# Optimization experiments

Hardware: AMD Instinct MI355X
Metric: run time of the kernel (lower is better)

The kernel has to match this reference:

```python
import jax, jax.numpy as jnp
import numpy as np

B, S, D, H = 4, 2048, 1024, 16
DK = D // H  # 64
EPS = 1e-6


def setup_inputs() -> dict:
    key = jax.random.key(0)
    ks = jax.random.split(key, 8)
    scale = 0.02
    return {
        "query": jax.random.normal(ks[0], (B, S, D), jnp.float32),
        "key": jax.random.normal(ks[1], (B, S, D), jnp.float32),
        "value": jax.random.normal(ks[2], (B, S, D), jnp.float32),
        "mask": jnp.zeros((B, 1, S, S), jnp.float32),  # additive mask
        "Wq": jax.random.normal(ks[3], (D, D), jnp.float32) * scale,
        "Wk": jax.random.normal(ks[4], (D, D), jnp.float32) * scale,
        "Wv": jax.random.normal(ks[5], (D, D), jnp.float32) * scale,
        "Wo": jax.random.normal(ks[6], (D, D), jnp.float32) * scale,
        "gamma": jnp.ones((D,), jnp.float32),
        "beta": jnp.zeros((D,), jnp.float32),
    }


def reference(query, key, value, mask, Wq, Wk, Wv, Wo, gamma, beta):
    residual = query
    # projections: [B,S,D] -> [B,H,S,dk]
    q = (query @ Wq).reshape(B, S, H, DK).transpose(0, 2, 1, 3)
    k = (key @ Wk).reshape(B, S, H, DK).transpose(0, 2, 1, 3)
    v = (value @ Wv).reshape(B, S, H, DK).transpose(0, 2, 1, 3)
    temperature = jnp.sqrt(jnp.asarray(DK, q.dtype))
    scores = jnp.einsum("bhqd,bhkd->bhqk", q, k) / temperature + mask
    p_attn = jax.nn.softmax(scores, axis=-1)  # dropout p=0 (eval)
    x = jnp.einsum("bhqk,bhkd->bhqd", p_attn, v)
    x = x.transpose(0, 2, 1, 3).reshape(B, S, D)
    x = x @ Wo
    y = residual + x
    mu = jnp.mean(y, axis=-1, keepdims=True)
    var = jnp.var(y, axis=-1, keepdims=True)
    return (y - mu) * jax.lax.rsqrt(var + EPS) * gamma + beta
```

## Files before the change

### kernel.cpp

```cpp
#include <hip/hip_runtime.h>
#include <string.h>

typedef unsigned short u16;
typedef __bf16 bf16x8 __attribute__((ext_vector_type(8)));
typedef float f32x4 __attribute__((ext_vector_type(4)));
typedef u16 us8 __attribute__((ext_vector_type(8)));
typedef u16 us4 __attribute__((ext_vector_type(4)));

#define DEVINL __device__ __forceinline__

static constexpr int Bn = 4, Sn = 2048, Dn = 1024, Hn = 16;
static constexpr float LOG2E = 1.4426950408889634f;

DEVINL u16 f2bf(float f) {
  __bf16 h = (__bf16)f;
  u16 u;
  memcpy(&u, &h, 2);
  return u;
}

DEVINL void gload16(const void* g, void* l) {
  __builtin_amdgcn_global_load_lds((const __attribute__((address_space(1))) void*)g,
                                   (__attribute__((address_space(3))) void*)l, 16, 0, 0);
}

DEVINL unsigned swz(unsigned row, unsigned kbyte) {
  return row * 128u + (kbyte ^ ((row & 7u) << 4));
}

DEVINL bf16x8 lds8(const u16* base, unsigned byteoff) {
  return *(const bf16x8*)((const char*)base + byteoff);
}

__global__ __launch_bounds__(256) void cvt_all(const float* __restrict__ q, const float* __restrict__ k,
                                               const float* __restrict__ v, const float* __restrict__ mask,
                                               u16* __restrict__ oq, u16* __restrict__ ok,
                                               u16* __restrict__ ov, int* __restrict__ flag) {
  int z = blockIdx.y;
  if (z == 3) {
    size_t i = ((size_t)blockIdx.x * 256 + threadIdx.x) * 4;
    float4 m = *(const float4*)(mask + i);
    bool nz = (m.x != 0.f) || (m.y != 0.f) || (m.z != 0.f) || (m.w != 0.f);
    if (nz) atomicOr(flag, 1);
    return;
  }
  const float* in = z == 0 ? q : (z == 1 ? k : v);
  u16* out = z == 0 ? oq : (z == 1 ? ok : ov);
  size_t i = ((size_t)blockIdx.x * 256 + threadIdx.x) * 8;
  float4 a = *(const float4*)(in + i);
  float4 b = *(const float4*)(in + i + 4);
  us8 o;
  o[0] = f2bf(a.x); o[1] = f2bf(a.y); o[2] = f2bf(a.z); o[3] = f2bf(a.w);
  o[4] = f2bf(b.x); o[5] = f2bf(b.y); o[6] = f2bf(b.z); o[7] = f2bf(b.w);
  *(us8*)(out + i) = o;
}

__global__ __launch_bounds__(256) void cvt_w_all(const float* __restrict__ w0, const float* __restrict__ w1,
                                                 const float* __restrict__ w2, const float* __restrict__ w3,
                                                 u16* __restrict__ t0, u16* __restrict__ t1,
                                                 u16* __restrict__ t2, u16* __restrict__ t3) {
  int z = blockIdx.z;
  const float* W = z == 0 ? w0 : (z == 1 ? w1 : (z == 2 ? w2 : w3));
  u16* Wt = z == 0 ? t0 : (z == 1 ? t1 : (z == 2 ? t2 : t3));
  __shared__ float T[32][33];
  int n0 = blockIdx.x * 32, k0 = blockIdx.y * 32;
  int tx = threadIdx.x & 31, ty = threadIdx.x >> 5;
#pragma unroll
  for (int r = 0; r < 4; r++)
    T[ty + r * 8][tx] = W[(size_t)(k0 + ty + r * 8) * 1024 + n0 + tx];
  __syncthreads();
#pragma unroll
  for (int r = 0; r < 4; r++)
    Wt[(size_t)(n0 + ty + r * 8) * 1024 + k0 + tx] = f2bf(T[tx][ty + r * 8]);
}

__global__ __launch_bounds__(256) void transpose_v(const u16* __restrict__ V, u16* __restrict__ Vt) {
  __shared__ u16 T[64][72];
  int s0 = blockIdx.x * 64;
  int b = blockIdx.y >> 4, h = blockIdx.y & 15;
  int tid = threadIdx.x;
#pragma unroll
  for (int it = 0; it < 2; it++) {
    int chunk = it * 256 + tid;
    int s = chunk >> 3, c = chunk & 7;
    us8 v = *(const us8*)&V[((size_t)(b * Sn + s0 + s)) * Dn + h * 64 + c * 8];
#pragma unroll
    for (int j = 0; j < 8; j++) T[c * 8 + j][s] = v[j];
  }
  __syncthreads();
#pragma unroll
  for (int it = 0; it < 2; it++) {
    int chunk = it * 256 + tid;
    int dk = chunk >> 3, c = chunk & 7;
    us8 o;
#pragma unroll
    for (int jj = 0; jj < 8; jj++) o[jj] = T[dk][(jj & 3) * 16 + c * 2 + (jj >> 2)];
    *(us8*)&Vt[((size_t)((b * Hn + h) * 64 + dk)) * Sn + s0 + c * 8] = o;
  }
}

template <int EPI>
DEVINL void gemm_body(const u16* __restrict__ A, const u16* __restrict__ Bt, void* __restrict__ Cout,
                      const float* __restrict__ resid, float alpha, u16* As, u16* Bs, int m0, int n0) {
  constexpr int K = 1024, N = 1024;
  int tid = threadIdx.x, w = tid >> 6, l = tid & 63;
  int wr = w >> 1, wc = w & 1;
  int l15 = l & 15, l4 = l >> 4;
  int lrow8 = l >> 3;
  int chunk = (l & 7) ^ (lrow8 & 7);

  f32x4 acc[4][4];
#pragma unroll
  for (int i = 0; i < 4; i++)
#pragma unroll
    for (int j = 0; j < 4; j++)
#pragma unroll
      for (int r = 0; r < 4; r++) acc[i][j][r] = 0.f;

  for (int kt = 0; kt < K; kt += 64) {
    __syncthreads();
#pragma unroll
    for (int c = 0; c < 4; c++) {
      int rowb = w * 32 + c * 8;
      int row = rowb + lrow8;
      gload16(&A[(size_t)(m0 + row) * K + kt + chunk * 8], &As[rowb * 64]);
      gload16(&Bt[(size_t)(n0 + row) * K + kt + chunk * 8], &Bs[rowb * 64]);
    }
    __syncthreads();
#pragma unroll
    for (int kk = 0; kk < 2; kk++) {
      bf16x8 af[4], bfr[4];
#pragma unroll
      for (int i = 0; i < 4; i++) {
        af[i] = lds8(As, swz(wr * 64 + i * 16 + l15, kk * 64 + l4 * 16));
        bfr[i] = lds8(Bs, swz(wc * 64 + i * 16 + l15, kk * 64 + l4 * 16));
      }
#pragma unroll
      for (int mi = 0; mi < 4; mi++)
#pragma unroll
        for (int ni = 0; ni < 4; ni++)
          acc[mi][ni] = __builtin_amdgcn_mfma_f32_16x16x32_bf16(af[mi], bfr[ni], acc[mi][ni], 0, 0, 0);
    }
  }

#pragma unroll
  for (int mi = 0; mi < 4; mi++)
#pragma unroll
    for (int ni = 0; ni < 4; ni++)
#pragma unroll
      for (int r = 0; r < 4; r++) {
        int row = m0 + wr * 64 + mi * 16 + l4 * 4 + r;
        int col = n0 + wc * 64 + ni * 16 + l15;
        float v = acc[mi][ni][r] * alpha;
        if constexpr (EPI == 0) {
          ((u16*)Cout)[(size_t)row * N + col] = f2bf(v);
        } else {
          ((float*)Cout)[(size_t)row * N + col] = v + resid[(size_t)row * N + col];
        }
      }
}

DEVINL void swizzled_tiles(int& m0, int& n0) {
  int lin = blockIdx.y * 8 + blockIdx.x;
  int sl = (lin & 7) * 64 + (lin >> 3);
  n0 = (sl & 7) * 128;
  m0 = (sl >> 3) * 128;
}

__global__ __launch_bounds__(256) void gemm_qkv(const u16* __restrict__ Aq, const u16* __restrict__ Ak,
                                                const u16* __restrict__ Av, const u16* __restrict__ Wtq,
                                                const u16* __restrict__ Wtk, const u16* __restrict__ Wtv,
                                                u16* __restrict__ Cq, u16* __restrict__ Ck,
                                                u16* __restrict__ Cv, float alphaq) {
  __shared__ u16 As[128 * 64];
  __shared__ u16 Bs[128 * 64];
  int z = blockIdx.z;
  const u16* A = z == 0 ? Aq : (z == 1 ? Ak : Av);
  const u16* Bt = z == 0 ? Wtq : (z == 1 ? Wtk : Wtv);
  u16* C = z == 0 ? Cq : (z == 1 ? Ck : Cv);
  float alpha = z == 0 ? alphaq : 1.0f;
  int m0, n0;
  swizzled_tiles(m0, n0);
  gemm_body<0>(A, Bt, C, nullptr, alpha, As, Bs, m0, n0);
}

__global__ __launch_bounds__(256) void gemm_o(const u16* __restrict__ A, const u16* __restrict__ Bt,
                                              float* __restrict__ Cout, const float* __restrict__ resid) {
  __shared__ u16 As[128 * 64];
  __shared__ u16 Bs[128 * 64];
  int m0, n0;
  swizzled_tiles(m0, n0);
  gemm_body<1>(A, Bt, Cout, resid, 1.0f, As, Bs, m0, n0);
}

__global__ __launch_bounds__(256) void attn_k(const u16* __restrict__ Qb, const u16* __restrict__ Kb,
                                              const u16* __restrict__ Vt, const float* __restrict__ mask,
                                              const int* __restrict__ flag, u16* __restrict__ Ob) {
  __shared__ u16 Ks[2][64 * 64];
  __shared__ u16 Vs[2][64 * 64];
  __shared__ u16 Pl[4 * 32 * 72];
  int tid = threadIdx.x, w = tid >> 6, l = tid & 63;
  int l15 = l & 15, l4 = l >> 4;
  int b = blockIdx.y >> 4, h = blockIdx.y & 15;
  int q0 = blockIdx.x * 128;
  int lrow8 = l >> 3;
  int chunk = (l & 7) ^ (lrow8 & 7);

  bf16x8 qf[2][2];
#pragma unroll
  for (int mi = 0; mi < 2; mi++)
#pragma unroll
    for (int kk = 0; kk < 2; kk++) {
      int row = q0 + w * 32 + mi * 16 + l15;
      qf[mi][kk] = *(const bf16x8*)&Qb[((size_t)(b * Sn + row)) * Dn + h * 64 + kk * 32 + l4 * 8];
    }

  float run_s[2][4];
  f32x4 acc[2][4];
#pragma unroll
  for (int mi = 0; mi < 2; mi++)
#pragma unroll
    for (int r = 0; r < 4; r++) run_s[mi][r] = 0.f;
#pragma unroll
  for (int mi = 0; mi < 2; mi++)
#pragma unroll
    for (int n = 0; n < 4; n++)
#pragma unroll
      for (int r = 0; r < 4; r++) acc[mi][n][r] = 0.f;

  int msk = *flag;
  u16* P = &Pl[w * 32 * 72];

  const size_t kbase = (size_t)b * Sn * Dn + h * 64 + chunk * 8;
  const size_t vbase = (size_t)(b * Hn + h) * 64 * Sn + chunk * 8;

#define STAGE(BUF, KV0)                                                          \
  {                                                                              \
    _Pragma("unroll") for (int c = 0; c < 2; c++) {                              \
      int rowb = w * 16 + c * 8;                                                 \
      int kv = rowb + lrow8;                                                     \
      gload16(&Kb[kbase + (size_t)(KV0 + kv) * Dn], &Ks[BUF][rowb * 64]);        \
      gload16(&Vt[vbase + (size_t)kv * Sn + KV0], &Vs[BUF][rowb * 64]);          \
    }                                                                            \
  }

  STAGE(0, 0);
  int buf = 0;

  for (int t = 0; t < 32; t++) {
    __syncthreads();
    if (t + 1 < 32) STAGE(buf ^ 1, (t + 1) * 64);

    f32x4 sc[2][4];
#pragma unroll
    for (int mi = 0; mi < 2; mi++)
#pragma unroll
      for (int n = 0; n < 4; n++)
#pragma unroll
        for (int r = 0; r < 4; r++) sc[mi][n][r] = 0.f;
#pragma unroll
    for (int kk = 0; kk < 2; kk++) {
      bf16x8 kf[4];
#pragma unroll
      for (int n = 0; n < 4; n++) kf[n] = lds8(Ks[buf], swz(n * 16 + l15, kk * 64 + l4 * 16));
#pragma unroll
      for (int mi = 0; mi < 2; mi++)
#pragma unroll
        for (int n = 0; n < 4; n++)
          sc[mi][n] = __builtin_amdgcn_mfma_f32_16x16x32_bf16(qf[mi][kk], kf[n], sc[mi][n], 0, 0, 0);
    }

    if (msk) {
      int kv0 = t * 64;
#pragma unroll
      for (int mi = 0; mi < 2; mi++)
#pragma unroll
        for (int n = 0; n < 4; n++)
#pragma unroll
          for (int r = 0; r < 4; r++) {
            int qrow = q0 + w * 32 + mi * 16 + l4 * 4 + r;
            int kcol = kv0 + n * 16 + l15;
            sc[mi][n][r] += mask[(size_t)b * Sn * Sn + (size_t)qrow * Sn + kcol] * LOG2E;
          }
    }

#pragma unroll
    for (int mi = 0; mi < 2; mi++)
#pragma unroll
      for (int r = 0; r < 4; r++) {
        us4 o;
#pragma unroll
        for (int n = 0; n < 4; n++) {
          float p = exp2f(sc[mi][n][r]);
          run_s[mi][r] += p;
          o[n] = f2bf(p);
        }
        *(us4*)&P[(mi * 16 + l4 * 4 + r) * 72 + l15 * 4] = o;
      }

#pragma unroll
    for (int kk = 0; kk < 2; kk++) {
      bf16x8 pa[2], vf[4];
#pragma unroll
      for (int mi = 0; mi < 2; mi++)
        pa[mi] = *(const bf16x8*)((const char*)P + (mi * 16 + l15) * 144 + kk * 64 + l4 * 16);
#pragma unroll
      for (int n = 0; n < 4; n++) vf[n] = lds8(Vs[buf], swz(n * 16 + l15, kk * 64 + l4 * 16));
#pragma unroll
      for (int mi = 0; mi < 2; mi++)
#pragma unroll
        for (int n = 0; n < 4; n++)
          acc[mi][n] = __builtin_amdgcn_mfma_f32_16x16x32_bf16(pa[mi], vf[n], acc[mi][n], 0, 0, 0);
    }
    buf ^= 1;
  }
#undef STAGE

#pragma unroll
  for (int mi = 0; mi < 2; mi++)
#pragma unroll
    for (int r = 0; r < 4; r++) {
      float rs = run_s[mi][r];
      rs += __shfl_xor(rs, 1);
      rs += __shfl_xor(rs, 2);
      rs += __shfl_xor(rs, 4);
      rs += __shfl_xor(rs, 8);
      float inv = 1.0f / rs;
      int row = q0 + w * 32 + mi * 16 + l4 * 4 + r;
#pragma unroll
      for (int n = 0; n < 4; n++) {
        int col = h * 64 + n * 16 + l15;
        Ob[((size_t)(b * Sn + row)) * Dn + col] = f2bf(acc[mi][n][r] * inv);
      }
    }
}

__global__ __launch_bounds__(256) void ln_k(const float* __restrict__ y, const float* __restrict__ gamma,
                                            const float* __restrict__ beta, float* __restrict__ out) {
  int row = blockIdx.x;
  int tid = threadIdx.x;
  const float* p = y + (size_t)row * 1024 + tid * 4;
  float4 v = *(const float4*)p;
  float s = v.x + v.y + v.z + v.w;
  float ss = v.x * v.x + v.y * v.y + v.z * v.z + v.w * v.w;
#pragma unroll
  for (int off = 1; off < 64; off <<= 1) {
    s += __shfl_xor(s, off);
    ss += __shfl_xor(ss, off);
  }
  __shared__ float rs_[4], rss_[4];
  int w = tid >> 6, l = tid & 63;
  if (l == 0) { rs_[w] = s; rss_[w] = ss; }
  __syncthreads();
  s = rs_[0] + rs_[1] + rs_[2] + rs_[3];
  ss = rss_[0] + rss_[1] + rss_[2] + rss_[3];
  float mean = s * (1.f / 1024.f);
  float var = ss * (1.f / 1024.f) - mean * mean;
  float rstd = rsqrtf(var + 1e-6f);
  float4 g = *(const float4*)(gamma + tid * 4);
  float4 bb = *(const float4*)(beta + tid * 4);
  float4 o;
  o.x = (v.x - mean) * rstd * g.x + bb.x;
  o.y = (v.y - mean) * rstd * g.y + bb.y;
  o.z = (v.z - mean) * rstd * g.z + bb.z;
  o.w = (v.w - mean) * rstd * g.w + bb.w;
  *(float4*)(out + (size_t)row * 1024 + tid * 4) = o;
}

extern "C" void kernel_launch(void* const* d_in, const int* in_sizes, int n_in,
                              void* d_out, int out_size, void* d_ws, size_t ws_size,
                              hipStream_t stream) {
  const float* query = (const float*)d_in[0];
  const float* key_ = (const float*)d_in[1];
  const float* value = (const float*)d_in[2];
  const float* mask = (const float*)d_in[3];
  const float* Wq = (const float*)d_in[4];
  const float* Wk = (const float*)d_in[5];
  const float* Wv = (const float*)d_in[6];
  const float* Wo = (const float*)d_in[7];
  const float* gamma = (const float*)d_in[8];
  const float* beta = (const float*)d_in[9];

  char* ws = (char*)d_ws;
  int* flag = (int*)ws;
  size_t off = 256;
  u16* Wtq = (u16*)(ws + off); off += (size_t)1024 * 1024 * 2;
  u16* Wtk = (u16*)(ws + off); off += (size_t)1024 * 1024 * 2;
  u16* Wtv = (u16*)(ws + off); off += (size_t)1024 * 1024 * 2;
  u16* Wto = (u16*)(ws + off); off += (size_t)1024 * 1024 * 2;
  const size_t TOK = (size_t)8192 * 1024;
  u16* Qb = (u16*)(ws + off); off += TOK * 2;
  u16* Kb = (u16*)(ws + off); off += TOK * 2;
  u16* Vb = (u16*)(ws + off); off += TOK * 2;
  u16* Vt = (u16*)(ws + off); off += TOK * 2;
  u16* Xq = (u16*)(ws + off); off += TOK * 2;
  u16* Xk = (u16*)(ws + off); off += TOK * 2;
  u16* Xv = (u16*)(ws + off); off += TOK * 2;
  u16* attnX = Xq;
  float* yb = (float*)Xk;

  hipMemsetAsync(flag, 0, 4, stream);

  cvt_all<<<dim3(4096, 4), 256, 0, stream>>>(query, key_, value, mask, Xq, Xk, Xv, flag);
  cvt_w_all<<<dim3(32, 32, 4), 256, 0, stream>>>(Wq, Wk, Wv, Wo, Wtq, Wtk, Wtv, Wto);

  gemm_qkv<<<dim3(8, 64, 3), 256, 0, stream>>>(Xq, Xk, Xv, Wtq, Wtk, Wtv, Qb, Kb, Vb,
                                               0.125f * LOG2E);

  transpose_v<<<dim3(32, 64), 256, 0, stream>>>(Vb, Vt);

  attn_k<<<dim3(16, 64), 256, 0, stream>>>(Qb, Kb, Vt, mask, flag, attnX);

  gemm_o<<<dim3(8, 64), 256, 0, stream>>>(attnX, Wto, yb, query);

  ln_k<<<8192, 256, 0, stream>>>(yb, gamma, beta, (float*)d_out);
}
```

Baseline: 433.8 us.

## Switch attention to 32x32 MFMA with transposed scores and register-only P

Rewrites the attention inner loop to use 32x32x16 bf16 MFMAs and computes the scores transposed (K times Q), so each lane holds one query column. The probabilities are packed to bf16 in registers with v_cvt_pk_bf16_f32 and rearranged with v_permlane32_swap, which removes the per-wave LDS staging buffer for P. The row sum becomes a single per-lane accumulator, the K/V load pointers are advanced incrementally, and the V transpose kernel now reads its output row contiguously. The aim is fewer LDS round trips and instructions per tile, at the cost of relying on the exact MFMA register layout being correct.

Measured after the change: 426.6 us. No clear change (-1.7%).

```diff
diff --git a/kernel.cpp b/kernel.cpp
--- a/kernel.cpp
+++ b/kernel.cpp
@@ -2,10 +2,13 @@
 #include <string.h>
 
 typedef unsigned short u16;
+typedef unsigned int u32;
 typedef __bf16 bf16x8 __attribute__((ext_vector_type(8)));
 typedef float f32x4 __attribute__((ext_vector_type(4)));
+typedef float f32x16 __attribute__((ext_vector_type(16)));
 typedef u16 us8 __attribute__((ext_vector_type(8)));
 typedef u16 us4 __attribute__((ext_vector_type(4)));
+typedef u32 uu4 __attribute__((ext_vector_type(4)));
 
 #define DEVINL __device__ __forceinline__
 
@@ -30,6 +33,16 @@
 
 DEVINL bf16x8 lds8(const u16* base, unsigned byteoff) {
   return *(const bf16x8*)((const char*)base + byteoff);
+}
+
+DEVINL u32 cvtpk(float a, float b) {
+  u32 r;
+  asm("v_cvt_pk_bf16_f32 %0, %1, %2" : "=v"(r) : "v"(a), "v"(b));
+  return r;
+}
+
+DEVINL void permswap(u32& x, u32& y) {
+  asm("v_permlane32_swap_b32 %0, %1" : "+v"(x), "+v"(y));
 }
 
 __global__ __launch_bounds__(256) void cvt_all(const float* __restrict__ q, const float* __restrict__ k,
@@ -92,9 +105,7 @@
   for (int it = 0; it < 2; it++) {
     int chunk = it * 256 + tid;
     int dk = chunk >> 3, c = chunk & 7;
-    us8 o;
-#pragma unroll
-    for (int jj = 0; jj < 8; jj++) o[jj] = T[dk][(jj & 3) * 16 + c * 2 + (jj >> 2)];
+    us8 o = *(const us8*)&T[dk][c * 8];
     *(us8*)&Vt[((size_t)((b * Hn + h) * 64 + dk)) * Sn + s0 + c * 8] = o;
   }
 }
@@ -198,141 +209,130 @@
                                               const int* __restrict__ flag, u16* __restrict__ Ob) {
   __shared__ u16 Ks[2][64 * 64];
   __shared__ u16 Vs[2][64 * 64];
-  __shared__ u16 Pl[4 * 32 * 72];
   int tid = threadIdx.x, w = tid >> 6, l = tid & 63;
-  int l15 = l & 15, l4 = l >> 4;
+  int l31 = l & 31, hi = l >> 5;
   int b = blockIdx.y >> 4, h = blockIdx.y & 15;
   int q0 = blockIdx.x * 128;
   int lrow8 = l >> 3;
   int chunk = (l & 7) ^ (lrow8 & 7);
 
-  bf16x8 qf[2][2];
-#pragma unroll
-  for (int mi = 0; mi < 2; mi++)
-#pragma unroll
-    for (int kk = 0; kk < 2; kk++) {
-      int row = q0 + w * 32 + mi * 16 + l15;
-      qf[mi][kk] = *(const bf16x8*)&Qb[((size_t)(b * Sn + row)) * Dn + h * 64 + kk * 32 + l4 * 8];
-    }
-
-  float run_s[2][4];
-  f32x4 acc[2][4];
-#pragma unroll
-  for (int mi = 0; mi < 2; mi++)
-#pragma unroll
-    for (int r = 0; r < 4; r++) run_s[mi][r] = 0.f;
-#pragma unroll
-  for (int mi = 0; mi < 2; mi++)
-#pragma unroll
-    for (int n = 0; n < 4; n++)
-#pragma unroll
-      for (int r = 0; r < 4; r++) acc[mi][n][r] = 0.f;
+  bf16x8 qf[4];
+  {
+    const u16* qp = &Qb[((size_t)(b * Sn + q0 + w * 32 + l31)) * Dn + h * 64 + hi * 8];
+#pragma unroll
+    for (int ks = 0; ks < 4; ks++) qf[ks] = *(const bf16x8*)(qp + ks * 16);
+  }
+
+  float run_s = 0.f;
+  f32x16 acc[2];
+#pragma unroll
+  for (int dt = 0; dt < 2; dt++)
+#pragma unroll
+    for (int r = 0; r < 16; r++) acc[dt][r] = 0.f;
 
   int msk = *flag;
-  u16* P = &Pl[w * 32 * 72];
-
-  const size_t kbase = (size_t)b * Sn * Dn + h * 64 + chunk * 8;
-  const size_t vbase = (size_t)(b * Hn + h) * 64 * Sn + chunk * 8;
-
-#define STAGE(BUF, KV0)                                                          \
-  {                                                                              \
-    _Pragma("unroll") for (int c = 0; c < 2; c++) {                              \
-      int rowb = w * 16 + c * 8;                                                 \
-      int kv = rowb + lrow8;                                                     \
-      gload16(&Kb[kbase + (size_t)(KV0 + kv) * Dn], &Ks[BUF][rowb * 64]);        \
-      gload16(&Vt[vbase + (size_t)kv * Sn + KV0], &Vs[BUF][rowb * 64]);          \
-    }                                                                            \
-  }
-
-  STAGE(0, 0);
+
+  const u16* kptr = Kb + (size_t)b * Sn * Dn + h * 64 + chunk * 8;
+  const u16* vptr = Vt + (size_t)(b * Hn + h) * 64 * Sn + chunk * 8;
+
+#define STAGE(BUF)                                                    \
+  {                                                                   \
+    _Pragma("unroll") for (int c = 0; c < 2; c++) {                   \
+      int rowb = w * 16 + c * 8;                                      \
+      int kv = rowb + lrow8;                                          \
+      gload16(kptr + (size_t)kv * Dn, &Ks[BUF][rowb * 64]);           \
+      gload16(vptr + (size_t)kv * Sn, &Vs[BUF][rowb * 64]);           \
+    }                                                                 \
+  }
+
+  STAGE(0);
+  kptr += (size_t)64 * Dn;
+  vptr += 64;
   int buf = 0;
 
   for (int t = 0; t < 32; t++) {
     __syncthreads();
-    if (t + 1 < 32) STAGE(buf ^ 1, (t + 1) * 64);
-
-    f32x4 sc[2][4];
-#pragma unroll
-    for (int mi = 0; mi < 2; mi++)
-#pragma unroll
-      for (int n = 0; n < 4; n++)
-#pragma unroll
-        for (int r = 0; r < 4; r++) sc[mi][n][r] = 0.f;
-#pragma unroll
-    for (int kk = 0; kk < 2; kk++) {
-      bf16x8 kf[4];
-#pragma unroll
-      for (int n = 0; n < 4; n++) kf[n] = lds8(Ks[buf], swz(n * 16 + l15, kk * 64 + l4 * 16));
-#pragma unroll
-      for (int mi = 0; mi < 2; mi++)
-#pragma unroll
-        for (int n = 0; n < 4; n++)
-          sc[mi][n] = __builtin_amdgcn_mfma_f32_16x16x32_bf16(qf[mi][kk], kf[n], sc[mi][n], 0, 0, 0);
+    if (t + 1 < 32) {
+      STAGE(buf ^ 1);
+      kptr += (size_t)64 * Dn;
+      vptr += 64;
+    }
+
+    f32x16 sc[2];
+#pragma unroll
+    for (int kvt = 0; kvt < 2; kvt++)
+#pragma unroll
+      for (int r = 0; r < 16; r++) sc[kvt][r] = 0.f;
+#pragma unroll
+    for (int ks = 0; ks < 4; ks++) {
+#pragma unroll
+      for (int kvt = 0; kvt < 2; kvt++) {
+        bf16x8 kf = lds8(Ks[buf], swz(kvt * 32 + l31, ks * 32 + hi * 16));
+        sc[kvt] = __builtin_amdgcn_mfma_f32_32x32x16_bf16(kf, qf[ks], sc[kvt], 0, 0, 0);
+      }
     }
 
     if (msk) {
-      int kv0 = t * 64;
-#pragma unroll
-      for (int mi = 0; mi < 2; mi++)
-#pragma unroll
-        for (int n = 0; n < 4; n++)
-#pragma unroll
-          for (int r = 0; r < 4; r++) {
-            int qrow = q0 + w * 32 + mi * 16 + l4 * 4 + r;
-            int kcol = kv0 + n * 16 + l15;
-            sc[mi][n][r] += mask[(size_t)b * Sn * Sn + (size_t)qrow * Sn + kcol] * LOG2E;
-          }
-    }
-
-#pragma unroll
-    for (int mi = 0; mi < 2; mi++)
-#pragma unroll
-      for (int r = 0; r < 4; r++) {
-        us4 o;
-#pragma unroll
-        for (int n = 0; n < 4; n++) {
-          float p = exp2f(sc[mi][n][r]);
-          run_s[mi][r] += p;
-          o[n] = f2bf(p);
+      const float* mp = &mask[((size_t)b * Sn + (q0 + w * 32 + l31)) * Sn + t * 64];
+#pragma unroll
+      for (int kvt = 0; kvt < 2; kvt++)
+#pragma unroll
+        for (int r = 0; r < 16; r++) {
+          int kvl = (r & 3) + 8 * (r >> 2) + 4 * hi;
+          sc[kvt][r] += mp[kvt * 32 + kvl] * LOG2E;
         }
-        *(us4*)&P[(mi * 16 + l4 * 4 + r) * 72 + l15 * 4] = o;
+    }
+
+#pragma unroll
+    for (int kvt = 0; kvt < 2; kvt++)
+#pragma unroll
+      for (int r = 0; r < 16; r++) {
+        float p = exp2f(sc[kvt][r]);
+        run_s += p;
+        sc[kvt][r] = p;
       }
 
-#pragma unroll
-    for (int kk = 0; kk < 2; kk++) {
-      bf16x8 pa[2], vf[4];
-#pragma unroll
-      for (int mi = 0; mi < 2; mi++)
-        pa[mi] = *(const bf16x8*)((const char*)P + (mi * 16 + l15) * 144 + kk * 64 + l4 * 16);
-#pragma unroll
-      for (int n = 0; n < 4; n++) vf[n] = lds8(Vs[buf], swz(n * 16 + l15, kk * 64 + l4 * 16));
-#pragma unroll
-      for (int mi = 0; mi < 2; mi++)
-#pragma unroll
-        for (int n = 0; n < 4; n++)
-          acc[mi][n] = __builtin_amdgcn_mfma_f32_16x16x32_bf16(pa[mi], vf[n], acc[mi][n], 0, 0, 0);
+    bf16x8 pa[4];
+#pragma unroll
+    for (int ks = 0; ks < 4; ks++) {
+      const f32x16& s = sc[ks >> 1];
+      int rb = (ks & 1) * 8;
+      u32 x0 = cvtpk(s[rb + 0], s[rb + 1]);
+      u32 y0 = cvtpk(s[rb + 4], s[rb + 5]);
+      u32 x1 = cvtpk(s[rb + 2], s[rb + 3]);
+      u32 y1 = cvtpk(s[rb + 6], s[rb + 7]);
+      permswap(x0, y0);
+      permswap(x1, y1);
+      uu4 wv;
+      wv[0] = x0; wv[1] = x1; wv[2] = y0; wv[3] = y1;
+      pa[ks] = *(bf16x8*)&wv;
+    }
+
+#pragma unroll
+    for (int ks = 0; ks < 4; ks++) {
+#pragma unroll
+      for (int dt = 0; dt < 2; dt++) {
+        bf16x8 vf = lds8(Vs[buf], swz(dt * 32 + l31, ks * 32 + hi * 16));
+        acc[dt] = __builtin_amdgcn_mfma_f32_32x32x16_bf16(pa[ks], vf, acc[dt], 0, 0, 0);
+      }
     }
     buf ^= 1;
   }
 #undef STAGE
 
-#pragma unroll
-  for (int mi = 0; mi < 2; mi++)
-#pragma unroll
-    for (int r = 0; r < 4; r++) {
-      float rs = run_s[mi][r];
-      rs += __shfl_xor(rs, 1);
-      rs += __shfl_xor(rs, 2);
-      rs += __shfl_xor(rs, 4);
-      rs += __shfl_xor(rs, 8);
-      float inv = 1.0f / rs;
-      int row = q0 + w * 32 + mi * 16 + l4 * 4 + r;
-#pragma unroll
-      for (int n = 0; n < 4; n++) {
-        int col = h * 64 + n * 16 + l15;
-        Ob[((size_t)(b * Sn + row)) * Dn + col] = f2bf(acc[mi][n][r] * inv);
-      }
-    }
+  run_s += __shfl_xor(run_s, 32);
+  float inv = 1.0f / run_s;
+#pragma unroll
+  for (int r = 0; r < 16; r++) {
+    int ql = (r & 3) + 8 * (r >> 2) + 4 * hi;
+    float invq = __shfl(inv, ql);
+    int row = q0 + w * 32 + ql;
+#pragma unroll
+    for (int dt = 0; dt < 2; dt++) {
+      int col = h * 64 + dt * 32 + l31;
+      Ob[((size_t)(b * Sn + row)) * Dn + col] = f2bf(acc[dt][r] * invq);
+    }
+  }
 }
 
 __global__ __launch_bounds__(256) void ln_k(const float* __restrict__ y, const float* __restrict__ gamma,
```
